# Kernel tuning notes

Measured on AMD Instinct MI355X. Metric: run time of the kernel, lower is better.

Reference implementation:

```python
import jax, jax.numpy as jnp
import numpy as np

K = 3        # kernel size
PAD = 1      # padding
DG = 16      # deformable groups
MAXR = 10.0  # max_residue_magnitude


def _lrelu(x):
    return jnp.where(x >= 0, x, 0.1 * x)


def _conv3(x, w, b):
    y = jax.lax.conv_general_dilated(x, w, (1, 1), 'SAME',
                                     dimension_numbers=('NCHW', 'OIHW', 'NCHW'))
    return y + b[None, :, None, None]


def _deform_conv2d(x, offset, mask, weight, bias):
    # x: [B,Cin,H,W]; offset: [B,2*DG*K*K,H,W]; mask: [B,DG*K*K,H,W]
    B, Cin, H, W = x.shape
    Cout = weight.shape[0]
    G, Cg, K2 = DG, Cin // DG, K * K
    off = offset.reshape(B, G, K2, 2, H, W)
    dy, dx = off[:, :, :, 0], off[:, :, :, 1]
    ky = jnp.repeat(jnp.arange(K), K).astype(x.dtype)   # [K2]
    kx = jnp.tile(jnp.arange(K), K).astype(x.dtype)
    hh = jnp.arange(H, dtype=x.dtype)
    ww = jnp.arange(W, dtype=x.dtype)
    # sampling positions [B,G,K2,H,W]
    py = dy + ky[None, None, :, None, None] + hh[None, None, None, :, None] - PAD
    px = dx + kx[None, None, :, None, None] + ww[None, None, None, None, :] - PAD
    y0 = jnp.floor(py)
    x0 = jnp.floor(px)
    wy1 = py - y0
    wx1 = px - x0
    xf = x.reshape(B, G, Cg, H * W)

    def gather(yi, xi, wgt):
        valid = (yi >= 0) & (yi <= H - 1) & (xi >= 0) & (xi <= W - 1)
        idx = (jnp.clip(yi, 0, H - 1).astype(jnp.int32) * W
               + jnp.clip(xi, 0, W - 1).astype(jnp.int32)).reshape(B, G, -1)
        vals = jnp.take_along_axis(
            xf, jnp.broadcast_to(idx[:, :, None, :], (B, G, Cg, idx.shape[-1])), axis=3)
        vals = vals.reshape(B, G, Cg, K2, H, W)
        w = (wgt * valid.astype(x.dtype))[:, :, None]  # [B,G,1,K2,H,W]
        return vals * w

    s = (gather(y0, x0, (1 - wy1) * (1 - wx1))
         + gather(y0, x0 + 1, (1 - wy1) * wx1)
         + gather(y0 + 1, x0, wy1 * (1 - wx1))
         + gather(y0 + 1, x0 + 1, wy1 * wx1))
    s = s * mask.reshape(B, G, K2, H, W)[:, :, None]
    wr = weight.reshape(Cout, G, Cg, K2)
    out = jnp.einsum('ogck,bgckhw->bohw', wr, s)
    return out + bias[None, :, None, None]


def setup_inputs() -> dict:
    key = jax.random.key(0)
    ks = jax.random.split(key, 16)
    B, Cin, Cout, H, W = 4, 128, 64, 96, 96
    Coff = 3 * Cout + 4  # 196
    stdv = 1.0 / np.sqrt(Cin * K * K)
    inp = {
        'x': jax.random.normal(ks[0], (B, Cin, H, W), jnp.float32),
        'extra_feat': jax.random.normal(ks[1], (B, 3 * Cout, H, W), jnp.float32),
        'flow_1': jax.random.normal(ks[2], (B, 2, H, W), jnp.float32),
        'flow_2': jax.random.normal(ks[3], (B, 2, H, W), jnp.float32),
        'weight': jax.random.uniform(ks[4], (Cout, Cin, K, K), jnp.float32, -stdv, stdv),
        'bias': jax.random.normal(ks[5], (Cout,), jnp.float32) * 0.01,
        'ow0': jax.random.normal(ks[6], (Cout, Coff, K, K), jnp.float32) * 0.02,
        'ob0': jnp.zeros((Cout,), jnp.float32),
        'ow1': jax.random.normal(ks[7], (Cout, Cout, K, K), jnp.float32) * 0.02,
        'ob1': jnp.zeros((Cout,), jnp.float32),
        'ow2': jax.random.normal(ks[8], (Cout, Cout, K, K), jnp.float32) * 0.02,
        'ob2': jnp.zeros((Cout,), jnp.float32),
        'ow3': jax.random.normal(ks[9], (27 * DG, Cout, K, K), jnp.float32) * 0.01,
        'ob3': jnp.zeros((27 * DG,), jnp.float32),
    }
    return inp


def reference(x, extra_feat, flow_1, flow_2, weight, bias,
              ow0, ob0, ow1, ob1, ow2, ob2, ow3, ob3):
    feat = jnp.concatenate([extra_feat, flow_1, flow_2], axis=1)
    h = _lrelu(_conv3(feat, ow0, ob0))
    h = _lrelu(_conv3(h, ow1, ob1))
    h = _lrelu(_conv3(h, ow2, ob2))
    out = _conv3(h, ow3, ob3)
    o1, o2, m = jnp.split(out, 3, axis=1)
    offs = MAXR * jnp.tanh(jnp.concatenate([o1, o2], axis=1))
    off1, off2 = jnp.split(offs, 2, axis=1)
    off1 = off1 + jnp.tile(flow_1[:, ::-1], (1, off1.shape[1] // 2, 1, 1))
    off2 = off2 + jnp.tile(flow_2[:, ::-1], (1, off2.shape[1] // 2, 1, 1))
    offset = jnp.concatenate([off1, off2], axis=1)
    mask = jax.nn.sigmoid(m)
    return _deform_conv2d(x, offset, mask, weight, bias)
```

## Files before the change

kernel.cpp:

```cpp
#include <hip/hip_runtime.h>
#include <math.h>

#define HW 9216
#define Hh 96
#define Ww 96
#define PHW 9604

typedef __attribute__((ext_vector_type(8))) short bh8;
typedef __attribute__((ext_vector_type(4))) short bh4;
typedef __attribute__((ext_vector_type(4))) float f32x4;

__device__ __forceinline__ short f2bf(float f) {
    union { float f; unsigned u; } v; v.f = f;
    unsigned r = v.u + 0x7FFFu + ((v.u >> 16) & 1u);
    return (short)(r >> 16);
}
__device__ __forceinline__ float bf2f(short s) {
    union { unsigned u; float f; } v; v.u = ((unsigned)(unsigned short)s) << 16;
    return v.f;
}

__global__ void zero_border(short* __restrict__ p, int C) {
    int i = blockIdx.x * 256 + threadIdx.x;
    int total = 4 * 388 * C;
    if (i >= total) return;
    int c = i % C;
    int r = i / C;
    int b = r / 388, pid = r - b * 388;
    int row, col;
    if (pid < 98)       { row = 0;  col = pid; }
    else if (pid < 196) { row = 97; col = pid - 98; }
    else if (pid < 292) { row = pid - 196 + 1; col = 0; }
    else                { row = pid - 292 + 1; col = 97; }
    p[((size_t)b * PHW + row * 98 + col) * C + c] = 0;
}

__global__ void pack_x1(const float* __restrict__ extra,
                        const float* __restrict__ f1,
                        const float* __restrict__ f2,
                        short* __restrict__ xp) {
    __shared__ float t[32][33];
    const int tid = threadIdx.x, tx = tid & 31, ty = tid >> 5;
    const int pt = blockIdx.x, ct = blockIdx.y, b = blockIdx.z;
#pragma unroll
    for (int j = 0; j < 4; ++j) {
        int ch = ct * 32 + ty + j * 8;
        int p = pt * 32 + tx;
        float v = 0.f;
        if (ch < 192)      v = extra[(b * 192 + ch) * HW + p];
        else if (ch < 194) v = f1[(b * 2 + ch - 192) * HW + p];
        else if (ch < 196) v = f2[(b * 2 + ch - 194) * HW + p];
        t[ty + j * 8][tx] = v;
    }
    __syncthreads();
#pragma unroll
    for (int j = 0; j < 4; ++j) {
        int pr = ty + j * 8;
        int p = pt * 32 + pr;
        int r = p / 96, c = p - r * 96;
        xp[((size_t)b * PHW + (r + 1) * 98 + (c + 1)) * 224 + ct * 32 + tx] =
            f2bf(t[tx][pr]);
    }
}

__global__ void pack_xd(const float* __restrict__ x, short* __restrict__ xd) {
    __shared__ float t[32][33];
    const int tid = threadIdx.x, tx = tid & 31, ty = tid >> 5;
    const int pt = blockIdx.x, ct = blockIdx.y, b = blockIdx.z;
#pragma unroll
    for (int j = 0; j < 4; ++j) {
        int ch = ct * 32 + ty + j * 8;
        t[ty + j * 8][tx] = x[((size_t)b * 128 + ch) * HW + pt * 32 + tx];
    }
    __syncthreads();
#pragma unroll
    for (int j = 0; j < 4; ++j) {
        int pr = ty + j * 8;
        xd[((size_t)b * HW + pt * 32 + pr) * 128 + ct * 32 + tx] = f2bf(t[tx][pr]);
    }
}

__global__ void prep_wconv(const float* __restrict__ w, short* __restrict__ wb,
                           int Cout, int Cin, int Copad, int CINP) {
    int i = blockIdx.x * 256 + threadIdx.x;
    int total = Copad * 9 * CINP;
    if (i >= total) return;
    int co = i / (9 * CINP);
    int r = i - co * 9 * CINP;
    int tap = r / CINP, ci = r - tap * CINP;
    float v = (co < Cout && ci < Cin) ? w[(co * Cin + ci) * 9 + tap] : 0.f;
    wb[i] = f2bf(v);
}

__global__ void prep_wd(const float* __restrict__ w, short* __restrict__ wbd) {
    int i = blockIdx.x * 256 + threadIdx.x;
    if (i >= 64 * 1152) return;
    int co = i / 1152, kd = i - co * 1152;
    int gt = kd >> 3, c = kd & 7;
    int g = gt / 9, tap = gt - g * 9;
    wbd[i] = f2bf(w[(co * 128 + g * 8 + c) * 9 + tap]);
}

template<int CINP, int KCH, int PIX, int MODE>
__launch_bounds__(256)
__global__ void conv_mfma(const short* __restrict__ xp,
                          const short* __restrict__ wb,
                          const float* __restrict__ bias,
                          void* __restrict__ o1, short* __restrict__ o2,
                          const float* __restrict__ flow1,
                          const float* __restrict__ flow2) {
    __shared__ __attribute__((aligned(16))) short smA[9 * 64 * 32];
    const int tid = threadIdx.x;
    const int lane = tid & 63, wv = tid >> 6;
    const int q = lane >> 4, l15 = lane & 15;
    const int b = blockIdx.y;
    const int co_base = blockIdx.z * 64;
    const int pix0 = blockIdx.x * (64 * PIX) + wv * (16 * PIX);

    int soh[PIX], sow[PIX];
    const short* bp[PIX];
#pragma unroll
    for (int s = 0; s < PIX; ++s) {
        int pixs = pix0 + s * 16;
        soh[s] = pixs / 96;
        sow[s] = pixs - soh[s] * 96;
        bp[s] = xp + ((size_t)b * PHW + soh[s] * 98 + sow[s] + l15) * CINP + q * 8;
    }

    const int sco = tid >> 2, sqq = tid & 3;
    const short* wsrc = wb + (size_t)(co_base + sco) * (9 * CINP) + sqq * 8;

    f32x4 acc[PIX][4];
#pragma unroll
    for (int s = 0; s < PIX; ++s)
#pragma unroll
        for (int t = 0; t < 4; ++t) acc[s][t] = (f32x4){0.f, 0.f, 0.f, 0.f};

    for (int p = 0; p < KCH; ++p) {
        __syncthreads();
        bh8 wtmp[9];
#pragma unroll
        for (int tap = 0; tap < 9; ++tap)
            wtmp[tap] = *(const bh8*)(wsrc + tap * CINP + p * 32);
#pragma unroll
        for (int tap = 0; tap < 9; ++tap)
            *(bh8*)&smA[tap * 2048 + sco * 32 + sqq * 8] = wtmp[tap];
        __syncthreads();
#pragma unroll
        for (int tap = 0; tap < 9; ++tap) {
            const int ky = tap / 3, kx = tap - (tap / 3) * 3;
            bh8 bf[PIX];
#pragma unroll
            for (int s = 0; s < PIX; ++s)
                bf[s] = *(const bh8*)(bp[s] + (ky * 98 + kx) * CINP + p * 32);
#pragma unroll
            for (int t = 0; t < 4; ++t) {
                bh8 af = *(const bh8*)&smA[tap * 2048 + (t * 16 + l15) * 32 + q * 8];
#pragma unroll
                for (int s = 0; s < PIX; ++s)
                    acc[s][t] = __builtin_amdgcn_mfma_f32_16x16x32_bf16(
                        af, bf[s], acc[s][t], 0, 0, 0);
            }
        }
    }

#pragma unroll
    for (int s = 0; s < PIX; ++s) {
        const int pix = pix0 + s * 16 + l15;
        if constexpr (MODE == 0) {
            short* outp = (short*)o1;
            size_t base = ((size_t)b * PHW + (soh[s] + 1) * 98 + sow[s] + l15 + 1) * 64;
#pragma unroll
            for (int t = 0; t < 4; ++t) {
                bh4 v4;
#pragma unroll
                for (int r = 0; r < 4; ++r) {
                    int co = co_base + t * 16 + q * 4 + r;
                    float v = acc[s][t][r] + bias[co];
                    v = (v >= 0.f) ? v : 0.1f * v;
                    v4[r] = f2bf(v);
                }
                *(bh4*)(outp + base + t * 16 + q * 4) = v4;
            }
        } else {
            float* oo = (float*)o1;
#pragma unroll
            for (int t = 0; t < 4; ++t) {
#pragma unroll
                for (int r = 0; r < 4; ++r) {
                    int ch = co_base + t * 16 + q * 4 + r;
                    if (ch < 432) {
                        float v = acc[s][t][r] + bias[ch];
                        if (ch < 288) {
                            float tt = 10.f * tanhf(v);
                            const float* fl = (ch < 144) ? flow1 : flow2;
                            float fv = fl[(b * 2 + (1 - (ch & 1))) * HW + pix];
                            oo[((size_t)b * 288 + ch) * HW + pix] = tt + fv;
                        } else {
                            o2[((size_t)b * 144 + (ch - 288)) * HW + pix] =
                                f2bf(1.f / (1.f + expf(-v)));
                        }
                    }
                }
            }
        }
    }
}

__launch_bounds__(256)
__global__ void deform_mfma(const short* __restrict__ xd,
                            const float* __restrict__ offs,
                            const short* __restrict__ maskb,
                            const short* __restrict__ wbd,
                            const float* __restrict__ bias,
                            float* __restrict__ out) {
    __shared__ float red[4][1024];
    const int tid = threadIdx.x;
    const int lane = tid & 63, wv = tid >> 6;
    const int q = lane >> 4, l15 = lane & 15;
    const int b = blockIdx.y;
    const int pix0 = blockIdx.x * 16;
    const int pix = pix0 + l15;
    const int h = pix / 96, w = pix - (pix / 96) * 96;

    const float* offp = offs + (size_t)b * 288 * HW + pix;
    const short* mp = maskb + (size_t)b * 144 * HW + pix;
    const short* xb = xd + (size_t)b * HW * 128;
    const short* ap = wbd + (size_t)l15 * 1152 + wv * 288 + q * 8;

    f32x4 acc[4];
#pragma unroll
    for (int t = 0; t < 4; ++t) acc[t] = (f32x4){0.f, 0.f, 0.f, 0.f};

#pragma unroll
    for (int i = 0; i < 9; ++i) {
        const int gt = wv * 36 + i * 4 + q;
        float dy = offp[(size_t)(2 * gt) * HW];
        float dx = offp[(size_t)(2 * gt + 1) * HW];
        float m  = bf2f(mp[(size_t)gt * HW]);
        int g = gt / 9, tap = gt - (gt / 9) * 9;
        float py = dy + (float)(tap / 3) + (float)h - 1.f;
        float px = dx + (float)(tap - (tap / 3) * 3) + (float)w - 1.f;
        float y0f = floorf(py), x0f = floorf(px);
        float wy1 = py - y0f, wx1 = px - x0f;
        float wy0 = 1.f - wy1, wx0 = 1.f - wx1;
        int y0 = (int)y0f, x0 = (int)x0f;
        int y1 = y0 + 1, x1 = x0 + 1;
        bool vy0 = (y0 >= 0) && (y0 < Hh), vy1 = (y1 >= 0) && (y1 < Hh);
        bool vx0 = (x0 >= 0) && (x0 < Ww), vx1 = (x1 >= 0) && (x1 < Ww);
        int cy0 = min(max(y0, 0), Hh - 1), cy1 = min(max(y1, 0), Hh - 1);
        int cx0 = min(max(x0, 0), Ww - 1), cx1 = min(max(x1, 0), Ww - 1);
        float w00 = wy0 * wx0 * ((vy0 && vx0) ? m : 0.f);
        float w01 = wy0 * wx1 * ((vy0 && vx1) ? m : 0.f);
        float w10 = wy1 * wx0 * ((vy1 && vx0) ? m : 0.f);
        float w11 = wy1 * wx1 * ((vy1 && vx1) ? m : 0.f);
        const short* cb = xb + g * 8;
        bh8 a00 = *(const bh8*)(cb + (size_t)(cy0 * 96 + cx0) * 128);
        bh8 a01 = *(const bh8*)(cb + (size_t)(cy0 * 96 + cx1) * 128);
        bh8 a10 = *(const bh8*)(cb + (size_t)(cy1 * 96 + cx0) * 128);
        bh8 a11 = *(const bh8*)(cb + (size_t)(cy1 * 96 + cx1) * 128);
        bh8 bf;
#pragma unroll
        for (int c = 0; c < 8; ++c) {
            float s = w00 * bf2f(a00[c]) + w01 * bf2f(a01[c])
                    + w10 * bf2f(a10[c]) + w11 * bf2f(a11[c]);
            bf[c] = f2bf(s);
        }
#pragma unroll
        for (int t = 0; t < 4; ++t) {
            bh8 af = *(const bh8*)(ap + (size_t)t * 16 * 1152 + i * 32);
            acc[t] = __builtin_amdgcn_mfma_f32_16x16x32_bf16(af, bf, acc[t], 0, 0, 0);
        }
    }

#pragma unroll
    for (int t = 0; t < 4; ++t)
#pragma unroll
        for (int r = 0; r < 4; ++r)
            red[wv][(t * 16 + q * 4 + r) * 16 + l15] = acc[t][r];
    __syncthreads();
    for (int e = tid; e < 1024; e += 256) {
        int co = e >> 4, pl = e & 15;
        float v = red[0][e] + red[1][e] + red[2][e] + red[3][e] + bias[co];
        out[((size_t)b * 64 + co) * HW + pix0 + pl] = v;
    }
}

extern "C" void kernel_launch(void* const* d_in, const int* in_sizes, int n_in,
                              void* d_out, int out_size, void* d_ws, size_t ws_size,
                              hipStream_t stream) {
    const float* x      = (const float*)d_in[0];
    const float* extra  = (const float*)d_in[1];
    const float* flow1  = (const float*)d_in[2];
    const float* flow2  = (const float*)d_in[3];
    const float* weight = (const float*)d_in[4];
    const float* bias   = (const float*)d_in[5];
    const float* ow0    = (const float*)d_in[6];
    const float* ob0    = (const float*)d_in[7];
    const float* ow1    = (const float*)d_in[8];
    const float* ob1    = (const float*)d_in[9];
    const float* ow2    = (const float*)d_in[10];
    const float* ob2    = (const float*)d_in[11];
    const float* ow3    = (const float*)d_in[12];
    const float* ob3    = (const float*)d_in[13];
    float* out = (float*)d_out;

    char* wsb = (char*)d_ws;
    short* xpad1 = (short*)wsb;   wsb += (size_t)4 * PHW * 224 * 2;
    short* hpa   = (short*)wsb;   wsb += (size_t)4 * PHW * 64 * 2;
    short* hpb   = (short*)wsb;   wsb += (size_t)4 * PHW * 64 * 2;
    float* offbuf  = (float*)wsb; wsb += (size_t)4 * 288 * HW * 4;
    short* maskbuf = (short*)wsb; wsb += (size_t)4 * 144 * HW * 2;
    short* xd      = (short*)wsb; wsb += (size_t)4 * HW * 128 * 2;
    short* wb0     = (short*)wsb; wsb += 64 * 9 * 224 * 2;
    short* wb1     = (short*)wsb; wsb += 64 * 9 * 64 * 2;
    short* wb2     = (short*)wsb; wsb += 64 * 9 * 64 * 2;
    short* wb3     = (short*)wsb; wsb += 448 * 9 * 64 * 2;
    short* wbd     = (short*)wsb;

    auto g1 = [](int n) { return dim3((n + 255) / 256); };
    zero_border<<<g1(4 * 388 * 224), 256, 0, stream>>>(xpad1, 224);
    zero_border<<<g1(4 * 388 * 64), 256, 0, stream>>>(hpa, 64);
    zero_border<<<g1(4 * 388 * 64), 256, 0, stream>>>(hpb, 64);
    pack_x1<<<dim3(288, 7, 4), 256, 0, stream>>>(extra, flow1, flow2, xpad1);
    pack_xd<<<dim3(288, 4, 4), 256, 0, stream>>>(x, xd);
    prep_wconv<<<g1(64 * 9 * 224), 256, 0, stream>>>(ow0, wb0, 64, 196, 64, 224);
    prep_wconv<<<g1(64 * 9 * 64), 256, 0, stream>>>(ow1, wb1, 64, 64, 64, 64);
    prep_wconv<<<g1(64 * 9 * 64), 256, 0, stream>>>(ow2, wb2, 64, 64, 64, 64);
    prep_wconv<<<g1(448 * 9 * 64), 256, 0, stream>>>(ow3, wb3, 432, 64, 448, 64);
    prep_wd<<<g1(64 * 1152), 256, 0, stream>>>(weight, wbd);

    conv_mfma<224, 7, 1, 0><<<dim3(144, 4, 1), 256, 0, stream>>>(
        xpad1, wb0, ob0, (void*)hpa, nullptr, nullptr, nullptr);
    conv_mfma<64, 2, 1, 0><<<dim3(144, 4, 1), 256, 0, stream>>>(
        hpa, wb1, ob1, (void*)hpb, nullptr, nullptr, nullptr);
    conv_mfma<64, 2, 1, 0><<<dim3(144, 4, 1), 256, 0, stream>>>(
        hpb, wb2, ob2, (void*)hpa, nullptr, nullptr, nullptr);
    conv_mfma<64, 2, 2, 2><<<dim3(72, 4, 7), 256, 0, stream>>>(
        hpa, wb3, ob3, (void*)offbuf, maskbuf, flow1, flow2);
    deform_mfma<<<dim3(576, 4), 256, 0, stream>>>(
        xd, offbuf, maskbuf, wbd, bias, out);
}
```

Baseline: 336.8 us.

## Merge prep kernels, add LDS-tiled conv4 GEMM, and relayout deform inputs

```diff
diff --git a/kernel.cpp b/kernel.cpp
--- a/kernel.cpp
+++ b/kernel.cpp
@@ -9,6 +9,7 @@
 typedef __attribute__((ext_vector_type(8))) short bh8;
 typedef __attribute__((ext_vector_type(4))) short bh4;
 typedef __attribute__((ext_vector_type(4))) float f32x4;
+typedef __attribute__((ext_vector_type(2))) float f32x2;
 
 __device__ __forceinline__ short f2bf(float f) {
     union { float f; unsigned u; } v; v.f = f;
@@ -20,10 +21,16 @@
     return v.f;
 }
 
-__global__ void zero_border(short* __restrict__ p, int C) {
+__global__ void zero_borders(short* __restrict__ xpad1,
+                             short* __restrict__ hpa,
+                             short* __restrict__ hpb) {
     int i = blockIdx.x * 256 + threadIdx.x;
-    int total = 4 * 388 * C;
-    if (i >= total) return;
+    const int n1 = 4 * 388 * 224, n2 = 4 * 388 * 64;
+    short* p; int C;
+    if (i < n1) { p = xpad1; C = 224; }
+    else if (i < n1 + n2) { p = hpa; C = 64; i -= n1; }
+    else if (i < n1 + 2 * n2) { p = hpb; C = 64; i -= n1 + n2; }
+    else return;
     int c = i % C;
     int r = i / C;
     int b = r / 388, pid = r - b * 388;
@@ -73,48 +80,71 @@
         t[ty + j * 8][tx] = x[((size_t)b * 128 + ch) * HW + pt * 32 + tx];
     }
     __syncthreads();
-#pragma unroll
-    for (int j = 0; j < 4; ++j) {
-        int pr = ty + j * 8;
-        xd[((size_t)b * HW + pt * 32 + pr) * 128 + ct * 32 + tx] = f2bf(t[tx][pr]);
-    }
-}
-
-__global__ void prep_wconv(const float* __restrict__ w, short* __restrict__ wb,
-                           int Cout, int Cin, int Copad, int CINP) {
+    if (tid < 128) {
+        int oct = tid >> 5, p = tid & 31;
+        int g = (ct * 32 + oct * 8) >> 3;
+        bh8 v;
+#pragma unroll
+        for (int c = 0; c < 8; ++c) v[c] = f2bf(t[oct * 8 + c][p]);
+        *(bh8*)&xd[(((size_t)b * 16 + g) * HW + pt * 32 + p) * 8] = v;
+    }
+}
+
+__global__ void prep_weights(const float* __restrict__ ow0, const float* __restrict__ ow1,
+                             const float* __restrict__ ow2, const float* __restrict__ ow3,
+                             const float* __restrict__ wd,
+                             short* __restrict__ wb0, short* __restrict__ wb1,
+                             short* __restrict__ wb2, short* __restrict__ wb3,
+                             short* __restrict__ wbd) {
     int i = blockIdx.x * 256 + threadIdx.x;
-    int total = Copad * 9 * CINP;
-    if (i >= total) return;
-    int co = i / (9 * CINP);
-    int r = i - co * 9 * CINP;
-    int tap = r / CINP, ci = r - tap * CINP;
-    float v = (co < Cout && ci < Cin) ? w[(co * Cin + ci) * 9 + tap] : 0.f;
-    wb[i] = f2bf(v);
-}
-
-__global__ void prep_wd(const float* __restrict__ w, short* __restrict__ wbd) {
-    int i = blockIdx.x * 256 + threadIdx.x;
-    if (i >= 64 * 1152) return;
-    int co = i / 1152, kd = i - co * 1152;
-    int gt = kd >> 3, c = kd & 7;
-    int g = gt / 9, tap = gt - g * 9;
-    wbd[i] = f2bf(w[(co * 128 + g * 8 + c) * 9 + tap]);
-}
-
-template<int CINP, int KCH, int PIX, int MODE>
+    const int n0 = 64 * 9 * 224, n1 = 64 * 9 * 64, n3 = 448 * 9 * 64, nd = 64 * 1152;
+    if (i < n0) {
+        int co = i / (9 * 224); int r = i - co * (9 * 224);
+        int tap = r / 224, ci = r - tap * 224;
+        wb0[i] = f2bf(ci < 196 ? ow0[(co * 196 + ci) * 9 + tap] : 0.f);
+        return;
+    }
+    i -= n0;
+    if (i < n1) {
+        int co = i / (9 * 64); int r = i - co * (9 * 64);
+        int tap = r / 64, ci = r - tap * 64;
+        wb1[i] = f2bf(ow1[(co * 64 + ci) * 9 + tap]);
+        return;
+    }
+    i -= n1;
+    if (i < n1) {
+        int co = i / (9 * 64); int r = i - co * (9 * 64);
+        int tap = r / 64, ci = r - tap * 64;
+        wb2[i] = f2bf(ow2[(co * 64 + ci) * 9 + tap]);
+        return;
+    }
+    i -= n1;
+    if (i < n3) {
+        int co = i / (9 * 64); int r = i - co * (9 * 64);
+        int tap = r / 64, ci = r - tap * 64;
+        wb3[i] = f2bf(co < 432 ? ow3[(co * 64 + ci) * 9 + tap] : 0.f);
+        return;
+    }
+    i -= n3;
+    if (i < nd) {
+        int co = i / 1152, kd = i - co * 1152;
+        int gt = kd >> 3, c = kd & 7;
+        int g = gt / 9, tap = gt - g * 9;
+        wbd[i] = f2bf(wd[(co * 128 + g * 8 + c) * 9 + tap]);
+    }
+}
+
+template<int CINP, int KCH, int PIX>
 __launch_bounds__(256)
 __global__ void conv_mfma(const short* __restrict__ xp,
                           const short* __restrict__ wb,
                           const float* __restrict__ bias,
-                          void* __restrict__ o1, short* __restrict__ o2,
-                          const float* __restrict__ flow1,
-                          const float* __restrict__ flow2) {
+                          short* __restrict__ o1) {
     __shared__ __attribute__((aligned(16))) short smA[9 * 64 * 32];
     const int tid = threadIdx.x;
     const int lane = tid & 63, wv = tid >> 6;
     const int q = lane >> 4, l15 = lane & 15;
     const int b = blockIdx.y;
-    const int co_base = blockIdx.z * 64;
     const int pix0 = blockIdx.x * (64 * PIX) + wv * (16 * PIX);
 
     int soh[PIX], sow[PIX];
@@ -128,7 +158,7 @@
     }
 
     const int sco = tid >> 2, sqq = tid & 3;
-    const short* wsrc = wb + (size_t)(co_base + sco) * (9 * CINP) + sqq * 8;
+    const short* wsrc = wb + (size_t)sco * (9 * CINP) + sqq * 8;
 
     f32x4 acc[PIX][4];
 #pragma unroll
@@ -166,40 +196,99 @@
 
 #pragma unroll
     for (int s = 0; s < PIX; ++s) {
-        const int pix = pix0 + s * 16 + l15;
-        if constexpr (MODE == 0) {
-            short* outp = (short*)o1;
-            size_t base = ((size_t)b * PHW + (soh[s] + 1) * 98 + sow[s] + l15 + 1) * 64;
-#pragma unroll
-            for (int t = 0; t < 4; ++t) {
-                bh4 v4;
-#pragma unroll
-                for (int r = 0; r < 4; ++r) {
-                    int co = co_base + t * 16 + q * 4 + r;
-                    float v = acc[s][t][r] + bias[co];
-                    v = (v >= 0.f) ? v : 0.1f * v;
-                    v4[r] = f2bf(v);
-                }
-                *(bh4*)(outp + base + t * 16 + q * 4) = v4;
+        size_t base = ((size_t)b * PHW + (soh[s] + 1) * 98 + sow[s] + l15 + 1) * 64;
+#pragma unroll
+        for (int t = 0; t < 4; ++t) {
+            bh4 v4;
+#pragma unroll
+            for (int r = 0; r < 4; ++r) {
+                int co = t * 16 + q * 4 + r;
+                float v = acc[s][t][r] + bias[co];
+                v = (v >= 0.f) ? v : 0.1f * v;
+                v4[r] = f2bf(v);
             }
-        } else {
-            float* oo = (float*)o1;
-#pragma unroll
-            for (int t = 0; t < 4; ++t) {
-#pragma unroll
-                for (int r = 0; r < 4; ++r) {
-                    int ch = co_base + t * 16 + q * 4 + r;
-                    if (ch < 432) {
-                        float v = acc[s][t][r] + bias[ch];
-                        if (ch < 288) {
-                            float tt = 10.f * tanhf(v);
-                            const float* fl = (ch < 144) ? flow1 : flow2;
-                            float fv = fl[(b * 2 + (1 - (ch & 1))) * HW + pix];
-                            oo[((size_t)b * 288 + ch) * HW + pix] = tt + fv;
-                        } else {
-                            o2[((size_t)b * 144 + (ch - 288)) * HW + pix] =
-                                f2bf(1.f / (1.f + expf(-v)));
-                        }
+            *(bh4*)(o1 + base + t * 16 + q * 4) = v4;
+        }
+    }
+}
+
+__launch_bounds__(256)
+__global__ void conv4_gemm(const short* __restrict__ xp,
+                           const short* __restrict__ wb,
+                           const float* __restrict__ bias,
+                           float* __restrict__ offp,
+                           short* __restrict__ maskb,
+                           const float* __restrict__ flow1,
+                           const float* __restrict__ flow2) {
+    __shared__ __attribute__((aligned(16))) short smA[64 * 40];
+    __shared__ __attribute__((aligned(16))) short smB[192 * 40];
+    const int tid = threadIdx.x;
+    const int lane = tid & 63, wv = tid >> 6;
+    const int q = lane >> 4, l15 = lane & 15;
+    const int pg = blockIdx.x;
+    const int b = blockIdx.y;
+    const int cob = blockIdx.z * 64;
+    const int r0 = pg * 2;
+
+    const int a_co = tid >> 2, a_ks = tid & 3;
+    const short* asrc = wb + (size_t)(cob + a_co) * 576 + a_ks * 8;
+
+    f32x4 acc[3][4];
+#pragma unroll
+    for (int pf = 0; pf < 3; ++pf)
+#pragma unroll
+        for (int cf = 0; cf < 4; ++cf) acc[pf][cf] = (f32x4){0.f, 0.f, 0.f, 0.f};
+
+    for (int ch = 0; ch < 18; ++ch) {
+        const int tap = ch >> 1, ci = (ch & 1) * 32;
+        const int ky = tap / 3, kx = tap - (tap / 3) * 3;
+        __syncthreads();
+        *(bh8*)&smA[a_co * 40 + a_ks * 8] = *(const bh8*)(asrc + tap * 64 + ci);
+#pragma unroll
+        for (int it = 0; it < 3; ++it) {
+            int id = it * 256 + tid;
+            int sp = id >> 2, ks = id & 3;
+            int srow = (sp >= 96) ? 1 : 0;
+            int scol = sp - srow * 96;
+            *(bh8*)&smB[sp * 40 + ks * 8] = *(const bh8*)&xp[
+                ((size_t)b * PHW + (r0 + srow + ky) * 98 + scol + kx) * 64 + ci + ks * 8];
+        }
+        __syncthreads();
+        bh8 bf[3], af[4];
+#pragma unroll
+        for (int pf = 0; pf < 3; ++pf)
+            bf[pf] = *(const bh8*)&smB[(wv * 48 + pf * 16 + l15) * 40 + q * 8];
+#pragma unroll
+        for (int cf = 0; cf < 4; ++cf)
+            af[cf] = *(const bh8*)&smA[(cf * 16 + l15) * 40 + q * 8];
+#pragma unroll
+        for (int pf = 0; pf < 3; ++pf)
+#pragma unroll
+            for (int cf = 0; cf < 4; ++cf)
+                acc[pf][cf] = __builtin_amdgcn_mfma_f32_16x16x32_bf16(
+                    af[cf], bf[pf], acc[pf][cf], 0, 0, 0);
+    }
+
+#pragma unroll
+    for (int pf = 0; pf < 3; ++pf) {
+        int local = wv * 48 + pf * 16 + l15;
+        int lrow = (local >= 96) ? 1 : 0;
+        int pix = (r0 + lrow) * 96 + (local - lrow * 96);
+#pragma unroll
+        for (int cf = 0; cf < 4; ++cf) {
+#pragma unroll
+            for (int r = 0; r < 4; ++r) {
+                int chn = cob + cf * 16 + q * 4 + r;
+                if (chn < 432) {
+                    float v = acc[pf][cf][r] + bias[chn];
+                    if (chn < 288) {
+                        float tt = 10.f * tanhf(v);
+                        const float* fl = (chn < 144) ? flow1 : flow2;
+                        float fv = fl[(b * 2 + (1 - (chn & 1))) * HW + pix];
+                        offp[(((size_t)b * 144 + (chn >> 1)) * HW + pix) * 2 + (chn & 1)] = tt + fv;
+                    } else {
+                        maskb[((size_t)b * 144 + (chn - 288)) * HW + pix] =
+                            f2bf(1.f / (1.f + expf(-v)));
                     }
                 }
             }
@@ -207,9 +296,8 @@
     }
 }
 
-__launch_bounds__(256)
 __global__ void deform_mfma(const short* __restrict__ xd,
-                            const float* __restrict__ offs,
+                            const float* __restrict__ offp,
                             const short* __restrict__ maskb,
                             const short* __restrict__ wbd,
                             const float* __restrict__ bias,
@@ -218,29 +306,37 @@
     const int tid = threadIdx.x;
     const int lane = tid & 63, wv = tid >> 6;
     const int q = lane >> 4, l15 = lane & 15;
-    const int b = blockIdx.y;
-    const int pix0 = blockIdx.x * 16;
+    const int blk = blockIdx.x;
+    const int xs = blk & 7, idx = blk >> 3;
+    const int b = xs >> 1;
+    const int pix0 = ((xs & 1) * 288 + idx) * 16;
     const int pix = pix0 + l15;
     const int h = pix / 96, w = pix - (pix / 96) * 96;
 
-    const float* offp = offs + (size_t)b * 288 * HW + pix;
+    const float* opp = offp + ((size_t)b * 144 * HW + pix) * 2;
     const short* mp = maskb + (size_t)b * 144 * HW + pix;
-    const short* xb = xd + (size_t)b * HW * 128;
+    const short* xb = xd + (size_t)b * 16 * HW * 8;
     const short* ap = wbd + (size_t)l15 * 1152 + wv * 288 + q * 8;
 
-    f32x4 acc[4];
-#pragma unroll
-    for (int t = 0; t < 4; ++t) acc[t] = (f32x4){0.f, 0.f, 0.f, 0.f};
-
+    f32x2 dxy[9];
+    float mk[9];
 #pragma unroll
     for (int i = 0; i < 9; ++i) {
         const int gt = wv * 36 + i * 4 + q;
-        float dy = offp[(size_t)(2 * gt) * HW];
-        float dx = offp[(size_t)(2 * gt + 1) * HW];
-        float m  = bf2f(mp[(size_t)gt * HW]);
-        int g = gt / 9, tap = gt - (gt / 9) * 9;
-        float py = dy + (float)(tap / 3) + (float)h - 1.f;
-        float px = dx + (float)(tap - (tap / 3) * 3) + (float)w - 1.f;
+        dxy[i] = *(const f32x2*)(opp + (size_t)gt * HW * 2);
+        mk[i] = bf2f(mp[(size_t)gt * HW]);
+    }
+
+    f32x4 acc[4];
+#pragma unroll
+    for (int t = 0; t < 4; ++t) acc[t] = (f32x4){0.f, 0.f, 0.f, 0.f};
+
+#pragma unroll
+    for (int i = 0; i < 9; ++i) {
+        const int gt = wv * 36 + i * 4 + q;
+        const int g = gt / 9, tap = gt - (gt / 9) * 9;
+        float py = dxy[i][0] + (float)(tap / 3) + (float)h - 1.f;
+        float px = dxy[i][1] + (float)(tap - (tap / 3) * 3) + (float)w - 1.f;
         float y0f = floorf(py), x0f = floorf(px);
         float wy1 = py - y0f, wx1 = px - x0f;
         float wy0 = 1.f - wy1, wx0 = 1.f - wx1;
@@ -250,15 +346,16 @@
         bool vx0 = (x0 >= 0) && (x0 < Ww), vx1 = (x1 >= 0) && (x1 < Ww);
         int cy0 = min(max(y0, 0), Hh - 1), cy1 = min(max(y1, 0), Hh - 1);
         int cx0 = min(max(x0, 0), Ww - 1), cx1 = min(max(x1, 0), Ww - 1);
+        float m = mk[i];
         float w00 = wy0 * wx0 * ((vy0 && vx0) ? m : 0.f);
         float w01 = wy0 * wx1 * ((vy0 && vx1) ? m : 0.f);
         float w10 = wy1 * wx0 * ((vy1 && vx0) ? m : 0.f);
         float w11 = wy1 * wx1 * ((vy1 && vx1) ? m : 0.f);
-        const short* cb = xb + g * 8;
-        bh8 a00 = *(const bh8*)(cb + (size_t)(cy0 * 96 + cx0) * 128);
-        bh8 a01 = *(const bh8*)(cb + (size_t)(cy0 * 96 + cx1) * 128);
-        bh8 a10 = *(const bh8*)(cb + (size_t)(cy1 * 96 + cx0) * 128);
-        bh8 a11 = *(const bh8*)(cb + (size_t)(cy1 * 96 + cx1) * 128);
+        const short* cb = xb + (size_t)g * HW * 8;
+        bh8 a00 = *(const bh8*)(cb + (size_t)(cy0 * 96 + cx0) * 8);
+        bh8 a01 = *(const bh8*)(cb + (size_t)(cy0 * 96 + cx1) * 8);
+        bh8 a10 = *(const bh8*)(cb + (size_t)(cy1 * 96 + cx0) * 8);
+        bh8 a11 = *(const bh8*)(cb + (size_t)(cy1 * 96 + cx1) * 8);
         bh8 bf;
 #pragma unroll
         for (int c = 0; c < 8; ++c) {
@@ -309,9 +406,9 @@
     short* xpad1 = (short*)wsb;   wsb += (size_t)4 * PHW * 224 * 2;
     short* hpa   = (short*)wsb;   wsb += (size_t)4 * PHW * 64 * 2;
     short* hpb   = (short*)wsb;   wsb += (size_t)4 * PHW * 64 * 2;
-    float* offbuf  = (float*)wsb; wsb += (size_t)4 * 288 * HW * 4;
+    float* offpair = (float*)wsb; wsb += (size_t)4 * 144 * HW * 2 * 4;
     short* maskbuf = (short*)wsb; wsb += (size_t)4 * 144 * HW * 2;
-    short* xd      = (short*)wsb; wsb += (size_t)4 * HW * 128 * 2;
+    short* xd      = (short*)wsb; wsb += (size_t)4 * 16 * HW * 8 * 2 + 32;
     short* wb0     = (short*)wsb; wsb += 64 * 9 * 224 * 2;
     short* wb1     = (short*)wsb; wsb += 64 * 9 * 64 * 2;
     short* wb2     = (short*)wsb; wsb += 64 * 9 * 64 * 2;
@@ -319,25 +416,16 @@
     short* wbd     = (short*)wsb;
 
     auto g1 = [](int n) { return dim3((n + 255) / 256); };
-    zero_border<<<g1(4 * 388 * 224), 256, 0, stream>>>(xpad1, 224);
-    zero_border<<<g1(4 * 388 * 64), 256, 0, stream>>>(hpa, 64);
-    zero_border<<<g1(4 * 388 * 64), 256, 0, stream>>>(hpb, 64);
+    zero_borders<<<g1(4 * 388 * 352), 256, 0, stream>>>(xpad1, hpa, hpb);
     pack_x1<<<dim3(288, 7, 4), 256, 0, stream>>>(extra, flow1, flow2, xpad1);
     pack_xd<<<dim3(288, 4, 4), 256, 0, stream>>>(x, xd);
-    prep_wconv<<<g1(64 * 9 * 224), 256, 0, stream>>>(ow0, wb0, 64, 196, 64, 224);
-    prep_wconv<<<g1(64 * 9 * 64), 256, 0, stream>>>(ow1, wb1, 64, 64, 64, 64);
-    prep_wconv<<<g1(64 * 9 * 64), 256, 0, stream>>>(ow2, wb2, 64, 64, 64, 64);
-    prep_wconv<<<g1(448 * 9 * 64), 256, 0, stream>>>(ow3, wb3, 432, 64, 448, 64);
-    prep_wd<<<g1(64 * 1152), 256, 0, stream>>>(weight, wbd);
-
-    conv_mfma<224, 7, 1, 0><<<dim3(144, 4, 1), 256, 0, stream>>>(
-        xpad1, wb0, ob0, (void*)hpa, nullptr, nullptr, nullptr);
-    conv_mfma<64, 2, 1, 0><<<dim3(144, 4, 1), 256, 0, stream>>>(
-        hpa, wb1, ob1, (void*)hpb, nullptr, nullptr, nullptr);
-    conv_mfma<64, 2, 1, 0><<<dim3(144, 4, 1), 256, 0, stream>>>(
-        hpb, wb2, ob2, (void*)hpa, nullptr, nullptr, nullptr);
-    conv_mfma<64, 2, 2, 2><<<dim3(72, 4, 7), 256, 0, stream>>>(
-        hpa, wb3, ob3, (void*)offbuf, maskbuf, flow1, flow2);
-    deform_mfma<<<dim3(576, 4), 256, 0, stream>>>(
-        xd, offbuf, maskbuf, wbd, bias, out);
-}
+    prep_weights<<<g1(534528), 256, 0, stream>>>(ow0, ow1, ow2, ow3, weight,
+                                                 wb0, wb1, wb2, wb3, wbd);
+
+    conv_mfma<224, 7, 1><<<dim3(144, 4), 256, 0, stream>>>(xpad1, wb0, ob0, hpa);
+    conv_mfma<64, 2, 1><<<dim3(144, 4), 256, 0, stream>>>(hpa, wb1, ob1, hpb);
+    conv_mfma<64, 2, 1><<<dim3(144, 4), 256, 0, stream>>>(hpb, wb2, ob2, hpa);
+    conv4_gemm<<<dim3(48, 4, 7), 256, 0, stream>>>(hpa, wb3, ob3, offpair,
+                                                   maskbuf, flow1, flow2);
+    deform_mfma<<<dim3(2304), 256, 0, stream>>>(xd, offpair, maskbuf, wbd, bias, out);
+}
```

Measured after the change: 314.8 us. -6.5%, faster.
